# Kernel tuning notes

Hardware: AMD Instinct MI355X
Metric: run time of the kernel (lower is better)

## Reference

```python
import jax, jax.numpy as jnp
import numpy as np

N, K = 8192, 64


def setup_inputs() -> dict:
    key = jax.random.key(0)
    k1, k2, k3 = jax.random.split(key, 3)
    F_ll = jax.random.normal(k1, (N, K), dtype=jnp.float32)
    F_ul = jax.random.normal(k2, (N, K), dtype=jnp.float32)
    Theta = jax.random.normal(k3, (N, N), dtype=jnp.float32)
    lambda_r = jnp.ones((), dtype=jnp.float32)
    return {"F_ll": F_ll, "F_ul": F_ul, "Theta": Theta, "lambda_r": lambda_r}


def reference(F_ll, F_ul, Theta, lambda_r):
    # term1 = trace(F_ll^T @ Theta @ F_ll) computed without forming the k x k product:
    # stream Theta once: (Theta @ F_ll) is n x k, then elementwise-dot with F_ll.
    term1 = jnp.sum((Theta @ F_ll) * F_ll)
    # term2 = lambda_r * trace(F_ll F_ll^T F_ul F_ul^T)
    #       = lambda_r * ||F_ul^T F_ll||_F^2 via cyclic trace identity -> only a k x k intermediate.
    G = jnp.einsum("nk,nj->kj", F_ul, F_ll)  # k x k
    term2 = lambda_r * jnp.sum(G * G)
    return term1 + term2
```

## Files before the change

### kernel.cpp

```cpp
#include <hip/hip_runtime.h>
#include <hip/hip_bf16.h>
#include <stdint.h>

#define N 8192
#define K 64

typedef __attribute__((ext_vector_type(8))) __bf16 bf16x8;
typedef __attribute__((ext_vector_type(4))) float f32x4;
typedef __attribute__((address_space(3))) uint8_t lds_u8;
typedef __attribute__((address_space(1))) const uint8_t glob_u8;


static __device__ __forceinline__ uint32_t f2bf(float f) {
  uint32_t x = __float_as_uint(f);
  return (x + 0x7FFFu + ((x >> 16) & 1u)) >> 16;
}

__global__ __launch_bounds__(256) void term2_kernel(const float* __restrict__ Fll,
                                                    const float* __restrict__ Ful,
                                                    float* __restrict__ P2,
                                                    ushort* __restrict__ W0) {
  __shared__ float sll[64][64];
  __shared__ float sul[64][64];
  const int t = threadIdx.x;
  const int j = t & 63, kq = t >> 6;
  const size_t r0 = (size_t)blockIdx.x * 64;

  for (int i = t; i < 1024; i += 256) {
    ((float4*)sll)[i] = ((const float4*)(Fll + r0 * K))[i];
    ((float4*)sul)[i] = ((const float4*)(Ful + r0 * K))[i];
  }
  __syncthreads();

  const float* sf = (const float*)sll;
#pragma unroll
  for (int h = 0; h < 2; ++h) {
    int f = t * 8 + h * 2048;
    uint32_t r[8];
#pragma unroll
    for (int e = 0; e < 8; ++e) r[e] = f2bf(sf[f + e]);
    uint4 o;
    o.x = r[0] | (r[1] << 16);
    o.y = r[2] | (r[3] << 16);
    o.z = r[4] | (r[5] << 16);
    o.w = r[6] | (r[7] << 16);
    *(uint4*)&W0[r0 * K + f] = o;
  }

  float acc[16];
#pragma unroll
  for (int m = 0; m < 16; ++m) acc[m] = 0.f;
  for (int r = 0; r < 64; ++r) {
    float fl = sll[r][j];
#pragma unroll
    for (int m = 0; m < 16; ++m) acc[m] += sul[r][kq * 16 + m] * fl;
  }
#pragma unroll
  for (int m = 0; m < 16; ++m)
    P2[(size_t)blockIdx.x * 4096 + (kq * 16 + m) * 64 + j] = acc[m];
}

__global__ __launch_bounds__(256) void term1_kernel(const float* __restrict__ Theta,
                                                    const ushort* __restrict__ Fb,
                                                    float* __restrict__ P1) {
  __shared__ float lds[2][16 * 260];
  const int t = threadIdx.x;
  const int lane = t & 63, wave = t >> 6;
  const int bi = blockIdx.x >> 5;
  const int bj = blockIdx.x & 31;
  const int i0 = bi * 64;
  const int jc0 = bj * 256;
  const int l15 = lane & 15, lg = lane >> 4;

  bf16x8 bfrag[4][2], afrag[4][2];
#pragma unroll
  for (int jf = 0; jf < 4; ++jf)
#pragma unroll
    for (int ks = 0; ks < 2; ++ks)
      bfrag[jf][ks] =
          *(const bf16x8*)&Fb[(size_t)(jc0 + wave * 64 + jf * 16 + l15) * K + ks * 32 + lg * 8];
#pragma unroll
  for (int s = 0; s < 4; ++s)
#pragma unroll
    for (int ks = 0; ks < 2; ++ks)
      afrag[s][ks] =
          *(const bf16x8*)&Fb[(size_t)(i0 + s * 16 + l15) * K + ks * 32 + lg * 8];

  float p = 0.f;

#define STAGE(s, buf)                                                                   \
  {                                                                                     \
    _Pragma("unroll") for (int q = 0; q < 4; ++q) {                                     \
      int row = wave + 4 * q;                                                           \
      const float* g = Theta + (size_t)(i0 + (s)*16 + row) * N + jc0 + lane * 4;        \
      float* l = &lds[buf][row * 260];                                                  \
      __builtin_amdgcn_global_load_lds((glob_u8*)g, (lds_u8*)l, 16, 0, 0);              \
    }                                                                                   \
  }

  STAGE(0, 0);
  __syncthreads();
#pragma unroll
  for (int s = 0; s < 4; ++s) {
    if (s < 3) STAGE(s + 1, (s + 1) & 1);
    f32x4 zero = {0.f, 0.f, 0.f, 0.f};
    f32x4 acc[4] = {zero, zero, zero, zero};
#pragma unroll
    for (int jf = 0; jf < 4; ++jf)
#pragma unroll
      for (int ks = 0; ks < 2; ++ks)
        acc[jf] = __builtin_amdgcn_mfma_f32_16x16x32_bf16(afrag[s][ks], bfrag[jf][ks],
                                                          acc[jf], 0, 0, 0);
    const float* lb = &lds[s & 1][0];
#pragma unroll
    for (int jf = 0; jf < 4; ++jf)
#pragma unroll
      for (int r = 0; r < 4; ++r)
        p += acc[jf][r] * lb[(lg * 4 + r) * 260 + wave * 64 + jf * 16 + l15];
    __syncthreads();
  }

#pragma unroll
  for (int off = 32; off > 0; off >>= 1) p += __shfl_down(p, off, 64);
  __shared__ float red[4];
  if (lane == 0) red[wave] = p;
  __syncthreads();
  if (t == 0) P1[blockIdx.x] = (red[0] + red[1]) + (red[2] + red[3]);
}

__global__ __launch_bounds__(256) void stage2_kernel(const float* __restrict__ P1,
                                                     const float* __restrict__ P2,
                                                     float* __restrict__ R1,
                                                     float* __restrict__ R2) {
  __shared__ float sg[4][64];
  const int t = threadIdx.x, b = blockIdx.x;
  const int l = t & 63, q = t >> 6;
  const int kj = b * 64 + l;
  float gp = 0.f;
  for (int blk = q * 32; blk < q * 32 + 32; ++blk) gp += P2[(size_t)blk * 4096 + kj];
  sg[q][l] = gp;
  float a = (t < 64) ? P1[b * 64 + t] : 0.f;
  __syncthreads();
  if (q == 0) {
    float g = (sg[0][l] + sg[1][l]) + (sg[2][l] + sg[3][l]);
    float r2 = g * g;
    float r1 = a;
#pragma unroll
    for (int off = 32; off > 0; off >>= 1) {
      r2 += __shfl_down(r2, off, 64);
      r1 += __shfl_down(r1, off, 64);
    }
    if (l == 0) {
      R1[b] = r1;
      R2[b] = r2;
    }
  }
}

__global__ void final_kernel(const float* __restrict__ R1, const float* __restrict__ R2,
                             const float* __restrict__ lam, float* __restrict__ out) {
  const int t = threadIdx.x;
  float r1 = R1[t], r2 = R2[t];
#pragma unroll
  for (int off = 32; off > 0; off >>= 1) {
    r1 += __shfl_down(r1, off, 64);
    r2 += __shfl_down(r2, off, 64);
  }
  if (t == 0) out[0] = r1 + lam[0] * r2;
}

extern "C" void kernel_launch(void* const* d_in, const int* in_sizes, int n_in,
                              void* d_out, int out_size, void* d_ws, size_t ws_size,
                              hipStream_t stream) {
  const float* Fll = (const float*)d_in[0];
  const float* Ful = (const float*)d_in[1];
  const float* Theta = (const float*)d_in[2];
  const float* lam = (const float*)d_in[3];
  float* out = (float*)d_out;

  char* ws = (char*)d_ws;
  ushort* W0 = (ushort*)ws;
  float* P1 = (float*)(ws + (1u << 20));
  float* P2 = (float*)(ws + (1u << 20) + (1u << 16));
  float* R1 = (float*)(ws + 0x310000u);
  float* R2 = (float*)(ws + 0x310400u);

  term2_kernel<<<128, 256, 0, stream>>>(Fll, Ful, P2, W0);
  term1_kernel<<<4096, 256, 0, stream>>>(Theta, W0, P1);
  stage2_kernel<<<64, 256, 0, stream>>>(P1, P2, R1, R2);
  final_kernel<<<1, 64, 0, stream>>>(R1, R2, lam, out);
}
```

Measured before the change: 64.90 us.

## Read Theta directly into registers matching transposed MFMA output layout, drop LDS staging

The term1 kernel now computes all 16 MFMA tiles up front, swapping the A and B operands so each lane's accumulator covers 4 consecutive columns of one row. It then reads Theta with direct float4 global loads that match this layout, instead of staging Theta through double-buffered LDS with global_load_lds and barriers. This removes the LDS traffic and the __syncthreads calls per stage. In exchange it uses more accumulator registers (64 floats), and the Theta loads are 16-byte accesses from 16 rows per wave, which may coalesce less well than the earlier row-contiguous staging.

After: 80.29 us. 1.24x slower.

```diff
diff --git a/kernel.cpp b/kernel.cpp
--- a/kernel.cpp
+++ b/kernel.cpp
@@ -7,8 +7,6 @@
 
 typedef __attribute__((ext_vector_type(8))) __bf16 bf16x8;
 typedef __attribute__((ext_vector_type(4))) float f32x4;
-typedef __attribute__((address_space(3))) uint8_t lds_u8;
-typedef __attribute__((address_space(1))) const uint8_t glob_u8;
 
 
 static __device__ __forceinline__ uint32_t f2bf(float f) {
@@ -63,61 +61,52 @@
 __global__ __launch_bounds__(256) void term1_kernel(const float* __restrict__ Theta,
                                                     const ushort* __restrict__ Fb,
                                                     float* __restrict__ P1) {
-  __shared__ float lds[2][16 * 260];
   const int t = threadIdx.x;
   const int lane = t & 63, wave = t >> 6;
   const int bi = blockIdx.x >> 5;
   const int bj = blockIdx.x & 31;
   const int i0 = bi * 64;
-  const int jc0 = bj * 256;
+  const int jc0 = bj * 256 + wave * 64;
   const int l15 = lane & 15, lg = lane >> 4;
 
-  bf16x8 bfrag[4][2], afrag[4][2];
+  bf16x8 afrag[4][2], bfrag[4][2];
 #pragma unroll
-  for (int jf = 0; jf < 4; ++jf)
+  for (int m = 0; m < 4; ++m)
 #pragma unroll
     for (int ks = 0; ks < 2; ++ks)
-      bfrag[jf][ks] =
-          *(const bf16x8*)&Fb[(size_t)(jc0 + wave * 64 + jf * 16 + l15) * K + ks * 32 + lg * 8];
+      afrag[m][ks] = *(const bf16x8*)&Fb[(size_t)(i0 + m * 16 + l15) * K + ks * 32 + lg * 8];
 #pragma unroll
-  for (int s = 0; s < 4; ++s)
+  for (int n = 0; n < 4; ++n)
 #pragma unroll
     for (int ks = 0; ks < 2; ++ks)
-      afrag[s][ks] =
-          *(const bf16x8*)&Fb[(size_t)(i0 + s * 16 + l15) * K + ks * 32 + lg * 8];
+      bfrag[n][ks] = *(const bf16x8*)&Fb[(size_t)(jc0 + n * 16 + l15) * K + ks * 32 + lg * 8];
+
+  f32x4 zero = {0.f, 0.f, 0.f, 0.f};
+  f32x4 acc[4][4];
+#pragma unroll
+  for (int m = 0; m < 4; ++m)
+#pragma unroll
+    for (int n = 0; n < 4; ++n)
+      acc[m][n] = zero;
+#pragma unroll
+  for (int m = 0; m < 4; ++m)
+#pragma unroll
+    for (int n = 0; n < 4; ++n)
+#pragma unroll
+      for (int ks = 0; ks < 2; ++ks)
+        acc[m][n] = __builtin_amdgcn_mfma_f32_16x16x32_bf16(bfrag[n][ks], afrag[m][ks],
+                                                            acc[m][n], 0, 0, 0);
 
   float p = 0.f;
-
-#define STAGE(s, buf)                                                                   \
-  {                                                                                     \
-    _Pragma("unroll") for (int q = 0; q < 4; ++q) {                                     \
-      int row = wave + 4 * q;                                                           \
-      const float* g = Theta + (size_t)(i0 + (s)*16 + row) * N + jc0 + lane * 4;        \
-      float* l = &lds[buf][row * 260];                                                  \
-      __builtin_amdgcn_global_load_lds((glob_u8*)g, (lds_u8*)l, 16, 0, 0);              \
-    }                                                                                   \
-  }
-
-  STAGE(0, 0);
-  __syncthreads();
 #pragma unroll
-  for (int s = 0; s < 4; ++s) {
-    if (s < 3) STAGE(s + 1, (s + 1) & 1);
-    f32x4 zero = {0.f, 0.f, 0.f, 0.f};
-    f32x4 acc[4] = {zero, zero, zero, zero};
+  for (int m = 0; m < 4; ++m) {
+    const float* base = Theta + (size_t)(i0 + m * 16 + l15) * N + jc0 + lg * 4;
 #pragma unroll
-    for (int jf = 0; jf < 4; ++jf)
-#pragma unroll
-      for (int ks = 0; ks < 2; ++ks)
-        acc[jf] = __builtin_amdgcn_mfma_f32_16x16x32_bf16(afrag[s][ks], bfrag[jf][ks],
-                                                          acc[jf], 0, 0, 0);
-    const float* lb = &lds[s & 1][0];
-#pragma unroll
-    for (int jf = 0; jf < 4; ++jf)
-#pragma unroll
-      for (int r = 0; r < 4; ++r)
-        p += acc[jf][r] * lb[(lg * 4 + r) * 260 + wave * 64 + jf * 16 + l15];
-    __syncthreads();
+    for (int n = 0; n < 4; ++n) {
+      float4 th = *(const float4*)(base + n * 16);
+      p += acc[m][n][0] * th.x + acc[m][n][1] * th.y + acc[m][n][2] * th.z +
+           acc[m][n][3] * th.w;
+    }
   }
 
 #pragma unroll
```

## Fuse term2 and term1 kernels, convert F_ll to bf16 inline

Applied to the files above, without the earlier changes.

Merges the separate term2 and term1 launches into one grid: the first 64 blocks compute the F_ul^T F_ll partials, each over 128 rows instead of 64, and the remaining blocks do the Theta streaming MFMA work. The term1 blocks now load fp32 F_ll directly and pack it to bf16 in registers, so the bf16 workspace copy and its dependency between launches go away. This removes one kernel launch and the serialization between them, in exchange for redundant fp32 loads and conversions of F_ll in every term1 block. The stage2 reduction loop is adjusted to the 64 P2 partials.

Result: slower. 93.64 us (+44.3%).

```diff
diff --git a/kernel.cpp b/kernel.cpp
--- a/kernel.cpp
+++ b/kernel.cpp
@@ -16,93 +16,103 @@
   return (x + 0x7FFFu + ((x >> 16) & 1u)) >> 16;
 }
 
-__global__ __launch_bounds__(256) void term2_kernel(const float* __restrict__ Fll,
+static __device__ __forceinline__ bf16x8 pack8(float4 a, float4 b) {
+  union {
+    ushort u[8];
+    bf16x8 v;
+  } r;
+  r.u[0] = (ushort)f2bf(a.x);
+  r.u[1] = (ushort)f2bf(a.y);
+  r.u[2] = (ushort)f2bf(a.z);
+  r.u[3] = (ushort)f2bf(a.w);
+  r.u[4] = (ushort)f2bf(b.x);
+  r.u[5] = (ushort)f2bf(b.y);
+  r.u[6] = (ushort)f2bf(b.z);
+  r.u[7] = (ushort)f2bf(b.w);
+  return r.v;
+}
+
+__global__ __launch_bounds__(256) void fused_kernel(const float* __restrict__ Theta,
+                                                    const float* __restrict__ Fll,
                                                     const float* __restrict__ Ful,
-                                                    float* __restrict__ P2,
-                                                    ushort* __restrict__ W0) {
-  __shared__ float sll[64][64];
-  __shared__ float sul[64][64];
+                                                    float* __restrict__ P1,
+                                                    float* __restrict__ P2) {
+  __shared__ float pool[2 * 16 * 260 + 8];
   const int t = threadIdx.x;
-  const int j = t & 63, kq = t >> 6;
-  const size_t r0 = (size_t)blockIdx.x * 64;
 
-  for (int i = t; i < 1024; i += 256) {
-    ((float4*)sll)[i] = ((const float4*)(Fll + r0 * K))[i];
-    ((float4*)sul)[i] = ((const float4*)(Ful + r0 * K))[i];
-  }
-  __syncthreads();
+  if (blockIdx.x < 64) {
+    float(*sll)[64] = (float(*)[64])pool;
+    float(*sul)[64] = (float(*)[64])(pool + 4096);
+    const int j = t & 63, kq = t >> 6;
+    float acc[16];
+#pragma unroll
+    for (int m = 0; m < 16; ++m) acc[m] = 0.f;
 
-  const float* sf = (const float*)sll;
+    for (int chunk = 0; chunk < 2; ++chunk) {
+      const size_t r0 = (size_t)blockIdx.x * 128 + chunk * 64;
+      for (int i = t; i < 1024; i += 256) {
+        ((float4*)sll)[i] = ((const float4*)(Fll + r0 * K))[i];
+        ((float4*)sul)[i] = ((const float4*)(Ful + r0 * K))[i];
+      }
+      __syncthreads();
+      for (int r = 0; r < 64; ++r) {
+        float fl = sll[r][j];
 #pragma unroll
-  for (int h = 0; h < 2; ++h) {
-    int f = t * 8 + h * 2048;
-    uint32_t r[8];
+        for (int m = 0; m < 16; ++m) acc[m] += sul[r][kq * 16 + m] * fl;
+      }
+      __syncthreads();
+    }
 #pragma unroll
-    for (int e = 0; e < 8; ++e) r[e] = f2bf(sf[f + e]);
-    uint4 o;
-    o.x = r[0] | (r[1] << 16);
-    o.y = r[2] | (r[3] << 16);
-    o.z = r[4] | (r[5] << 16);
-    o.w = r[6] | (r[7] << 16);
-    *(uint4*)&W0[r0 * K + f] = o;
+    for (int m = 0; m < 16; ++m)
+      P2[(size_t)blockIdx.x * 4096 + (kq * 16 + m) * 64 + j] = acc[m];
+    return;
   }
 
-  float acc[16];
-#pragma unroll
-  for (int m = 0; m < 16; ++m) acc[m] = 0.f;
-  for (int r = 0; r < 64; ++r) {
-    float fl = sll[r][j];
-#pragma unroll
-    for (int m = 0; m < 16; ++m) acc[m] += sul[r][kq * 16 + m] * fl;
-  }
-#pragma unroll
-  for (int m = 0; m < 16; ++m)
-    P2[(size_t)blockIdx.x * 4096 + (kq * 16 + m) * 64 + j] = acc[m];
-}
-
-__global__ __launch_bounds__(256) void term1_kernel(const float* __restrict__ Theta,
-                                                    const ushort* __restrict__ Fb,
-                                                    float* __restrict__ P1) {
-  __shared__ float lds[2][16 * 260];
-  const int t = threadIdx.x;
+  const int bid = blockIdx.x - 64;
   const int lane = t & 63, wave = t >> 6;
-  const int bi = blockIdx.x >> 5;
-  const int bj = blockIdx.x & 31;
+  const int bi = bid >> 5;
+  const int bj = bid & 31;
   const int i0 = bi * 64;
   const int jc0 = bj * 256;
   const int l15 = lane & 15, lg = lane >> 4;
 
-  bf16x8 bfrag[4][2], afrag[4][2];
+  float* lds0 = pool;
+  float* lds1 = pool + 16 * 260;
+
+#define STAGE(s, lbuf)                                                              \
+  {                                                                                 \
+    _Pragma("unroll") for (int q = 0; q < 4; ++q) {                                 \
+      int row = wave + 4 * q;                                                       \
+      const float* g = Theta + (size_t)(i0 + (s)*16 + row) * N + jc0 + lane * 4;    \
+      float* l = (lbuf) + row * 260;                                                \
+      __builtin_amdgcn_global_load_lds((glob_u8*)g, (lds_u8*)l, 16, 0, 0);          \
+    }                                                                               \
+  }
+
+  STAGE(0, lds0);
+
+  bf16x8 afrag[4][2], bfrag[4][2];
 #pragma unroll
-  for (int jf = 0; jf < 4; ++jf)
+  for (int m = 0; m < 4; ++m)
 #pragma unroll
-    for (int ks = 0; ks < 2; ++ks)
-      bfrag[jf][ks] =
-          *(const bf16x8*)&Fb[(size_t)(jc0 + wave * 64 + jf * 16 + l15) * K + ks * 32 + lg * 8];
+    for (int ks = 0; ks < 2; ++ks) {
+      const float* ar = Fll + (size_t)(i0 + m * 16 + l15) * K + ks * 32 + lg * 8;
+      afrag[m][ks] = pack8(*(const float4*)ar, *(const float4*)(ar + 4));
+    }
 #pragma unroll
-  for (int s = 0; s < 4; ++s)
+  for (int n = 0; n < 4; ++n)
 #pragma unroll
-    for (int ks = 0; ks < 2; ++ks)
-      afrag[s][ks] =
-          *(const bf16x8*)&Fb[(size_t)(i0 + s * 16 + l15) * K + ks * 32 + lg * 8];
+    for (int ks = 0; ks < 2; ++ks) {
+      const float* br = Fll + (size_t)(jc0 + wave * 64 + n * 16 + l15) * K + ks * 32 + lg * 8;
+      bfrag[n][ks] = pack8(*(const float4*)br, *(const float4*)(br + 4));
+    }
 
   float p = 0.f;
-
-#define STAGE(s, buf)                                                                   \
-  {                                                                                     \
-    _Pragma("unroll") for (int q = 0; q < 4; ++q) {                                     \
-      int row = wave + 4 * q;                                                           \
-      const float* g = Theta + (size_t)(i0 + (s)*16 + row) * N + jc0 + lane * 4;        \
-      float* l = &lds[buf][row * 260];                                                  \
-      __builtin_amdgcn_global_load_lds((glob_u8*)g, (lds_u8*)l, 16, 0, 0);              \
-    }                                                                                   \
-  }
-
-  STAGE(0, 0);
   __syncthreads();
 #pragma unroll
   for (int s = 0; s < 4; ++s) {
-    if (s < 3) STAGE(s + 1, (s + 1) & 1);
+    float* cur = (s & 1) ? lds1 : lds0;
+    if (s < 3) STAGE(s + 1, (s & 1) ? lds0 : lds1);
     f32x4 zero = {0.f, 0.f, 0.f, 0.f};
     f32x4 acc[4] = {zero, zero, zero, zero};
 #pragma unroll
@@ -111,12 +121,11 @@
       for (int ks = 0; ks < 2; ++ks)
         acc[jf] = __builtin_amdgcn_mfma_f32_16x16x32_bf16(afrag[s][ks], bfrag[jf][ks],
                                                           acc[jf], 0, 0, 0);
-    const float* lb = &lds[s & 1][0];
 #pragma unroll
     for (int jf = 0; jf < 4; ++jf)
 #pragma unroll
       for (int r = 0; r < 4; ++r)
-        p += acc[jf][r] * lb[(lg * 4 + r) * 260 + wave * 64 + jf * 16 + l15];
+        p += acc[jf][r] * cur[(lg * 4 + r) * 260 + wave * 64 + jf * 16 + l15];
     __syncthreads();
   }
 
@@ -125,7 +134,7 @@
   __shared__ float red[4];
   if (lane == 0) red[wave] = p;
   __syncthreads();
-  if (t == 0) P1[blockIdx.x] = (red[0] + red[1]) + (red[2] + red[3]);
+  if (t == 0) P1[bid] = (red[0] + red[1]) + (red[2] + red[3]);
 }
 
 __global__ __launch_bounds__(256) void stage2_kernel(const float* __restrict__ P1,
@@ -137,7 +146,7 @@
   const int l = t & 63, q = t >> 6;
   const int kj = b * 64 + l;
   float gp = 0.f;
-  for (int blk = q * 32; blk < q * 32 + 32; ++blk) gp += P2[(size_t)blk * 4096 + kj];
+  for (int blk = q * 16; blk < q * 16 + 16; ++blk) gp += P2[(size_t)blk * 4096 + kj];
   sg[q][l] = gp;
   float a = (t < 64) ? P1[b * 64 + t] : 0.f;
   __syncthreads();
@@ -179,14 +188,12 @@
   float* out = (float*)d_out;
 
   char* ws = (char*)d_ws;
-  ushort* W0 = (ushort*)ws;
-  float* P1 = (float*)(ws + (1u << 20));
-  float* P2 = (float*)(ws + (1u << 20) + (1u << 16));
-  float* R1 = (float*)(ws + 0x310000u);
-  float* R2 = (float*)(ws + 0x310400u);
+  float* P1 = (float*)ws;
+  float* P2 = (float*)(ws + 0x10000u);
+  float* R1 = (float*)(ws + 0x120000u);
+  float* R2 = (float*)(ws + 0x120400u);
 
-  term2_kernel<<<128, 256, 0, stream>>>(Fll, Ful, P2, W0);
-  term1_kernel<<<4096, 256, 0, stream>>>(Theta, W0, P1);
+  fused_kernel<<<4160, 256, 0, stream>>>(Theta, Fll, Ful, P1, P2);
   stage2_kernel<<<64, 256, 0, stream>>>(P1, P2, R1, R2);
   final_kernel<<<1, 64, 0, stream>>>(R1, R2, lam, out);
 }
```

## Deepen Theta prefetch, merge final reduction via atomic counter, split term2 finer

Applied to the files above, without the earlier changes.

The term1 kernel now issues two Theta stages up front and keeps two loads in flight, using explicit vmcnt waits and raw barriers in place of full __syncthreads. This is meant to hide global-to-LDS latency behind the MFMA work. The final reduction kernel is removed: the last stage2 block, detected with an atomic counter, does the final sum, saving one launch. term2 runs 256 blocks of 32 rows instead of 128 blocks of 64 for more parallelism, at the cost of a larger partial buffer and more work in stage2.

Result: slower. 87.11 us (+34.2%).

```diff
diff --git a/kernel.cpp b/kernel.cpp
--- a/kernel.cpp
+++ b/kernel.cpp
@@ -19,23 +19,25 @@
 __global__ __launch_bounds__(256) void term2_kernel(const float* __restrict__ Fll,
                                                     const float* __restrict__ Ful,
                                                     float* __restrict__ P2,
-                                                    ushort* __restrict__ W0) {
-  __shared__ float sll[64][64];
-  __shared__ float sul[64][64];
+                                                    ushort* __restrict__ W0,
+                                                    unsigned* __restrict__ cnt) {
+  __shared__ float sll[32][64];
+  __shared__ float sul[32][64];
   const int t = threadIdx.x;
   const int j = t & 63, kq = t >> 6;
-  const size_t r0 = (size_t)blockIdx.x * 64;
-
-  for (int i = t; i < 1024; i += 256) {
+  const size_t r0 = (size_t)blockIdx.x * 32;
+
+  if (blockIdx.x == 0 && t == 0) *cnt = 0u;
+
+  for (int i = t; i < 512; i += 256) {
     ((float4*)sll)[i] = ((const float4*)(Fll + r0 * K))[i];
     ((float4*)sul)[i] = ((const float4*)(Ful + r0 * K))[i];
   }
   __syncthreads();
 
   const float* sf = (const float*)sll;
-#pragma unroll
-  for (int h = 0; h < 2; ++h) {
-    int f = t * 8 + h * 2048;
+  {
+    int f = t * 8;
     uint32_t r[8];
 #pragma unroll
     for (int e = 0; e < 8; ++e) r[e] = f2bf(sf[f + e]);
@@ -50,7 +52,7 @@
   float acc[16];
 #pragma unroll
   for (int m = 0; m < 16; ++m) acc[m] = 0.f;
-  for (int r = 0; r < 64; ++r) {
+  for (int r = 0; r < 32; ++r) {
     float fl = sll[r][j];
 #pragma unroll
     for (int m = 0; m < 16; ++m) acc[m] += sul[r][kq * 16 + m] * fl;
@@ -72,37 +74,43 @@
   const int jc0 = bj * 256;
   const int l15 = lane & 15, lg = lane >> 4;
 
-  bf16x8 bfrag[4][2], afrag[4][2];
-#pragma unroll
-  for (int jf = 0; jf < 4; ++jf)
+#define STAGE(s, buf)                                                                \
+  {                                                                                  \
+    _Pragma("unroll") for (int q = 0; q < 4; ++q) {                                  \
+      int row = wave + 4 * q;                                                        \
+      const float* g = Theta + (size_t)(i0 + (s)*16 + row) * N + jc0 + lane * 4;     \
+      float* l = &lds[buf][row * 260];                                               \
+      __builtin_amdgcn_global_load_lds((glob_u8*)g, (lds_u8*)l, 16, 0, 0);           \
+    }                                                                                \
+  }
+
+  STAGE(0, 0);
+
+  bf16x8 afrag[4][2], bfrag[4][2];
+#pragma unroll
+  for (int m = 0; m < 4; ++m)
 #pragma unroll
     for (int ks = 0; ks < 2; ++ks)
-      bfrag[jf][ks] =
-          *(const bf16x8*)&Fb[(size_t)(jc0 + wave * 64 + jf * 16 + l15) * K + ks * 32 + lg * 8];
-#pragma unroll
-  for (int s = 0; s < 4; ++s)
+      afrag[m][ks] = *(const bf16x8*)&Fb[(size_t)(i0 + m * 16 + l15) * K + ks * 32 + lg * 8];
+#pragma unroll
+  for (int n = 0; n < 4; ++n)
 #pragma unroll
     for (int ks = 0; ks < 2; ++ks)
-      afrag[s][ks] =
-          *(const bf16x8*)&Fb[(size_t)(i0 + s * 16 + l15) * K + ks * 32 + lg * 8];
+      bfrag[n][ks] =
+          *(const bf16x8*)&Fb[(size_t)(jc0 + wave * 64 + n * 16 + l15) * K + ks * 32 + lg * 8];
+
+  STAGE(1, 1);
 
   float p = 0.f;
-
-#define STAGE(s, buf)                                                                   \
-  {                                                                                     \
-    _Pragma("unroll") for (int q = 0; q < 4; ++q) {                                     \
-      int row = wave + 4 * q;                                                           \
-      const float* g = Theta + (size_t)(i0 + (s)*16 + row) * N + jc0 + lane * 4;        \
-      float* l = &lds[buf][row * 260];                                                  \
-      __builtin_amdgcn_global_load_lds((glob_u8*)g, (lds_u8*)l, 16, 0, 0);              \
-    }                                                                                   \
-  }
-
-  STAGE(0, 0);
-  __syncthreads();
 #pragma unroll
   for (int s = 0; s < 4; ++s) {
-    if (s < 3) STAGE(s + 1, (s + 1) & 1);
+    if (s < 3)
+      asm volatile("s_waitcnt vmcnt(4)" ::: "memory");
+    else
+      asm volatile("s_waitcnt vmcnt(0)" ::: "memory");
+    __builtin_amdgcn_s_barrier();
+    __builtin_amdgcn_sched_barrier(0);
+
     f32x4 zero = {0.f, 0.f, 0.f, 0.f};
     f32x4 acc[4] = {zero, zero, zero, zero};
 #pragma unroll
@@ -111,13 +119,18 @@
       for (int ks = 0; ks < 2; ++ks)
         acc[jf] = __builtin_amdgcn_mfma_f32_16x16x32_bf16(afrag[s][ks], bfrag[jf][ks],
                                                           acc[jf], 0, 0, 0);
-    const float* lb = &lds[s & 1][0];
+    const float* cur = &lds[s & 1][0];
 #pragma unroll
     for (int jf = 0; jf < 4; ++jf)
 #pragma unroll
       for (int r = 0; r < 4; ++r)
-        p += acc[jf][r] * lb[(lg * 4 + r) * 260 + wave * 64 + jf * 16 + l15];
-    __syncthreads();
+        p += acc[jf][r] * cur[(lg * 4 + r) * 260 + wave * 64 + jf * 16 + l15];
+
+    if (s < 3) {
+      __builtin_amdgcn_sched_barrier(0);
+      __builtin_amdgcn_s_barrier();
+      if (s < 2) STAGE(s + 2, s & 1);
+    }
   }
 
 #pragma unroll
@@ -130,14 +143,18 @@
 
 __global__ __launch_bounds__(256) void stage2_kernel(const float* __restrict__ P1,
                                                      const float* __restrict__ P2,
+                                                     const float* __restrict__ lam,
+                                                     float* __restrict__ out,
                                                      float* __restrict__ R1,
-                                                     float* __restrict__ R2) {
+                                                     float* __restrict__ R2,
+                                                     unsigned* __restrict__ cnt) {
   __shared__ float sg[4][64];
+  __shared__ unsigned is_last;
   const int t = threadIdx.x, b = blockIdx.x;
   const int l = t & 63, q = t >> 6;
   const int kj = b * 64 + l;
   float gp = 0.f;
-  for (int blk = q * 32; blk < q * 32 + 32; ++blk) gp += P2[(size_t)blk * 4096 + kj];
+  for (int blk = q * 64; blk < q * 64 + 64; ++blk) gp += P2[(size_t)blk * 4096 + kj];
   sg[q][l] = gp;
   float a = (t < 64) ? P1[b * 64 + t] : 0.f;
   __syncthreads();
@@ -155,18 +172,22 @@
       R2[b] = r2;
     }
   }
-}
-
-__global__ void final_kernel(const float* __restrict__ R1, const float* __restrict__ R2,
-                             const float* __restrict__ lam, float* __restrict__ out) {
-  const int t = threadIdx.x;
-  float r1 = R1[t], r2 = R2[t];
-#pragma unroll
-  for (int off = 32; off > 0; off >>= 1) {
-    r1 += __shfl_down(r1, off, 64);
-    r2 += __shfl_down(r2, off, 64);
-  }
-  if (t == 0) out[0] = r1 + lam[0] * r2;
+  if (t == 0) {
+    __threadfence();
+    unsigned old = atomicAdd(cnt, 1u);
+    __threadfence();
+    is_last = (old == 63u) ? 1u : 0u;
+  }
+  __syncthreads();
+  if (is_last && t < 64) {
+    float r1 = R1[t], r2 = R2[t];
+#pragma unroll
+    for (int off = 32; off > 0; off >>= 1) {
+      r1 += __shfl_down(r1, off, 64);
+      r2 += __shfl_down(r2, off, 64);
+    }
+    if (t == 0) out[0] = r1 + lam[0] * r2;
+  }
 }
 
 extern "C" void kernel_launch(void* const* d_in, const int* in_sizes, int n_in,
@@ -182,11 +203,11 @@
   ushort* W0 = (ushort*)ws;
   float* P1 = (float*)(ws + (1u << 20));
   float* P2 = (float*)(ws + (1u << 20) + (1u << 16));
-  float* R1 = (float*)(ws + 0x310000u);
-  float* R2 = (float*)(ws + 0x310400u);
-
-  term2_kernel<<<128, 256, 0, stream>>>(Fll, Ful, P2, W0);
+  float* R1 = (float*)(ws + 0x510000u);
+  float* R2 = (float*)(ws + 0x510400u);
+  unsigned* cnt = (unsigned*)(ws + 0x510800u);
+
+  term2_kernel<<<256, 256, 0, stream>>>(Fll, Ful, P2, W0, cnt);
   term1_kernel<<<4096, 256, 0, stream>>>(Theta, W0, P1);
-  stage2_kernel<<<64, 256, 0, stream>>>(P1, P2, R1, R2);
-  final_kernel<<<1, 64, 0, stream>>>(R1, R2, lam, out);
-}
+  stage2_kernel<<<64, 256, 0, stream>>>(P1, P2, lam, out, R1, R2, cnt);
+}
```
